# Optimization experiments

Measured on AMD Instinct MI355X. Metric: run time of the kernel, lower is better.

The kernel has to match this reference:

```python
import jax, jax.numpy as jnp
import numpy as np

B, S, C = 16, 512, 512
T = 4096  # mel_max_len


def setup_inputs() -> dict:
    key = jax.random.key(0)
    k1, k2 = jax.random.split(key)
    durations = jax.random.randint(k1, (B, S), 0, 16, dtype=jnp.int32)
    enc_out = jax.random.normal(k2, (B, S, C), dtype=jnp.float32)
    return {"durations": durations, "enc_out": enc_out, "mel_max_len": T}


def reference(durations, enc_out, mel_max_len):
    # regulate_len with pace=1.0 and fixed mel_max_len (jit-static output length)
    pace = 1.0
    dtype = enc_out.dtype
    reps = (durations.astype(jnp.float32) / pace + 0.5).astype(jnp.int32)  # [B,S]
    dec_lens = reps.sum(axis=1)  # [B]
    # padded cumulative sums: [B, S+1]
    reps_cumsum = jnp.concatenate(
        [jnp.zeros((reps.shape[0], 1), reps.dtype), jnp.cumsum(reps, axis=1)], axis=1
    ).astype(dtype)[:, None, :]  # [B,1,S+1]
    range_ = jnp.arange(mel_max_len, dtype=dtype)[None, :, None]  # [1,T,1]
    mult = ((reps_cumsum[:, :, :-1] <= range_) & (reps_cumsum[:, :, 1:] > range_)).astype(dtype)  # [B,T,S]
    enc_rep = jnp.einsum('bts,bsc->btc', mult, enc_out)  # [B,T,C]
    dec_lens = jnp.minimum(dec_lens, mel_max_len)
    return enc_rep, dec_lens, reps.astype(jnp.float32)
```

## Files before the change

### kernel.cpp

```cpp
#include <hip/hip_runtime.h>

#define B_ 16
#define S_ 512
#define C_ 512
#define T_ 4096

typedef float f32x4 __attribute__((ext_vector_type(4)));

__global__ void __launch_bounds__(S_) regulate_scan_map_kernel(
    const int* __restrict__ dur,
    int* __restrict__ map,
    float* __restrict__ dec_out,
    float* __restrict__ reps_out)
{
    const int b    = blockIdx.x;
    const int s    = threadIdx.x;
    const int lane = s & 63;
    const int wid  = s >> 6;

    __shared__ int wsum[8];

    const int rep = dur[b * S_ + s];
    reps_out[b * S_ + s] = (float)rep;

    int x = rep;
    #pragma unroll
    for (int off = 1; off < 64; off <<= 1) {
        int y = __shfl_up(x, off, 64);
        if (lane >= off) x += y;
    }
    if (lane == 63) wsum[wid] = x;
    __syncthreads();

    int prefix = 0, total = 0;
    #pragma unroll
    for (int w = 0; w < 8; ++w) {
        int v = wsum[w];
        if (w < wid) prefix += v;
        total += v;
    }

    const int incl = prefix + x;
    const int excl = incl - rep;

    int start = excl < T_ ? excl : T_;
    int end   = incl < T_ ? incl : T_;
    int* __restrict__ m = map + (size_t)b * T_;
    for (int t = start; t < end; ++t) m[t] = s;

    const int tot_c = total < T_ ? total : T_;
    for (int t = tot_c + s; t < T_; t += S_) m[t] = -1;

    if (s == 0) dec_out[b] = (float)tot_c;
}

__global__ void __launch_bounds__(256) regulate_gather_kernel(
    const float* __restrict__ enc,
    const int* __restrict__ map,
    float* __restrict__ out)
{
    const int lin     = blockIdx.x;
    const int per     = gridDim.x >> 3;
    const int logical = (lin & 7) * per + (lin >> 3);

    const int b      = logical >> 10;
    const int tchunk = logical & 1023;
    const int row    = threadIdx.x >> 6;
    const int lane   = threadIdx.x & 63;
    const int t      = (tchunk << 2) + row;

    const int s = map[(size_t)b * T_ + t];

    f32x4 v0 = (f32x4)(0.f), v1 = (f32x4)(0.f);
    if (s >= 0) {
        const f32x4* __restrict__ rp =
            (const f32x4*)(enc + ((size_t)b * S_ + (size_t)s) * C_);
        v0 = rp[lane];
        v1 = rp[lane + 64];
    }
    f32x4* __restrict__ orow =
        (f32x4*)(out + ((size_t)b * T_ + (size_t)t) * C_);
    __builtin_nontemporal_store(v0, orow + lane);
    __builtin_nontemporal_store(v1, orow + lane + 64);
}

extern "C" void kernel_launch(void* const* d_in, const int* in_sizes, int n_in,
                              void* d_out, int out_size, void* d_ws, size_t ws_size,
                              hipStream_t stream)
{
    const int*   dur = (const int*)d_in[0];
    const float* enc = (const float*)d_in[1];

    float* out      = (float*)d_out;
    float* enc_rep  = out;
    float* dec_out  = out + (size_t)B_ * T_ * C_;
    float* reps_out = dec_out + B_;

    int* map = (int*)d_ws;

    regulate_scan_map_kernel<<<B_, S_, 0, stream>>>(dur, map, dec_out, reps_out);
    regulate_gather_kernel<<<(B_ * T_) / 4, 256, 0, stream>>>(enc, map, enc_rep);
}
```

Baseline: 32.49 us.

## Fuse duration scan into gather kernel, recomputing prefix sums per block

Removes the separate scan/map kernel and the workspace map by having every gather block redo the 512-entry prefix scan over its batch's durations (two per thread) and build a 4-entry row-to-source map in LDS. This drops one kernel launch and the serialized scan-then-gather dependency, including the map write and read through global memory. In exchange each of the 16K blocks does redundant scan work and a block-wide barrier before issuing its loads. The durations are small and likely cache-resident.

```diff
diff --git a/kernel.cpp b/kernel.cpp
--- a/kernel.cpp
+++ b/kernel.cpp
@@ -7,23 +7,33 @@
 
 typedef float f32x4 __attribute__((ext_vector_type(4)));
 
-__global__ void __launch_bounds__(S_) regulate_scan_map_kernel(
+__global__ void __launch_bounds__(256) regulate_fused_kernel(
     const int* __restrict__ dur,
-    int* __restrict__ map,
+    const float* __restrict__ enc,
+    float* __restrict__ out,
     float* __restrict__ dec_out,
     float* __restrict__ reps_out)
 {
-    const int b    = blockIdx.x;
-    const int s    = threadIdx.x;
-    const int lane = s & 63;
-    const int wid  = s >> 6;
+    const int lin     = blockIdx.x;
+    const int logical = (lin & 7) * (gridDim.x >> 3) + (lin >> 3);
 
-    __shared__ int wsum[8];
+    const int b      = logical >> 10;
+    const int tchunk = logical & 1023;
+    const int t0     = tchunk << 2;
 
-    const int rep = dur[b * S_ + s];
-    reps_out[b * S_ + s] = (float)rep;
+    const int tid  = threadIdx.x;
+    const int lane = tid & 63;
+    const int wid  = tid >> 6;
 
-    int x = rep;
+    __shared__ int wsum[4];
+    __shared__ int lds_map[4];
+
+    if (tid < 4) lds_map[tid] = -1;
+
+    const int2 d  = *(const int2*)(dur + b * S_ + (tid << 1));
+    const int pair = d.x + d.y;
+
+    int x = pair;
     #pragma unroll
     for (int off = 1; off < 64; off <<= 1) {
         int y = __shfl_up(x, off, 64);
@@ -34,42 +44,32 @@
 
     int prefix = 0, total = 0;
     #pragma unroll
-    for (int w = 0; w < 8; ++w) {
+    for (int w = 0; w < 4; ++w) {
         int v = wsum[w];
         if (w < wid) prefix += v;
         total += v;
     }
 
-    const int incl = prefix + x;
-    const int excl = incl - rep;
+    const int incl_pair = prefix + x;
+    const int excl0 = incl_pair - pair;
+    const int incl0 = excl0 + d.x;
+    const int incl1 = incl_pair;
 
-    int start = excl < T_ ? excl : T_;
-    int end   = incl < T_ ? incl : T_;
-    int* __restrict__ m = map + (size_t)b * T_;
-    for (int t = start; t < end; ++t) m[t] = s;
+    #pragma unroll
+    for (int j = 0; j < 4; ++j) {
+        const int t = t0 + j;
+        if (t >= excl0 && t < incl0) lds_map[j] = (tid << 1);
+        if (t >= incl0 && t < incl1) lds_map[j] = (tid << 1) | 1;
+    }
 
-    const int tot_c = total < T_ ? total : T_;
-    for (int t = tot_c + s; t < T_; t += S_) m[t] = -1;
+    if (tchunk == 0) {
+        *(float2*)(reps_out + b * S_ + (tid << 1)) =
+            make_float2((float)d.x, (float)d.y);
+        if (tid == 0) dec_out[b] = (float)(total < T_ ? total : T_);
+    }
+    __syncthreads();
 
-    if (s == 0) dec_out[b] = (float)tot_c;
-}
-
-__global__ void __launch_bounds__(256) regulate_gather_kernel(
-    const float* __restrict__ enc,
-    const int* __restrict__ map,
-    float* __restrict__ out)
-{
-    const int lin     = blockIdx.x;
-    const int per     = gridDim.x >> 3;
-    const int logical = (lin & 7) * per + (lin >> 3);
-
-    const int b      = logical >> 10;
-    const int tchunk = logical & 1023;
-    const int row    = threadIdx.x >> 6;
-    const int lane   = threadIdx.x & 63;
-    const int t      = (tchunk << 2) + row;
-
-    const int s = map[(size_t)b * T_ + t];
+    const int s = lds_map[wid];
 
     f32x4 v0 = (f32x4)(0.f), v1 = (f32x4)(0.f);
     if (s >= 0) {
@@ -78,10 +78,10 @@
         v0 = rp[lane];
         v1 = rp[lane + 64];
     }
-    f32x4* __restrict__ orow =
-        (f32x4*)(out + ((size_t)b * T_ + (size_t)t) * C_);
-    __builtin_nontemporal_store(v0, orow + lane);
-    __builtin_nontemporal_store(v1, orow + lane + 64);
+    f32x4* __restrict__ op =
+        (f32x4*)(out + ((size_t)b * T_ + (size_t)(t0 + wid)) * C_);
+    __builtin_nontemporal_store(v0, op + lane);
+    __builtin_nontemporal_store(v1, op + lane + 64);
 }
 
 extern "C" void kernel_launch(void* const* d_in, const int* in_sizes, int n_in,
@@ -96,8 +96,6 @@
     float* dec_out  = out + (size_t)B_ * T_ * C_;
     float* reps_out = dec_out + B_;
 
-    int* map = (int*)d_ws;
-
-    regulate_scan_map_kernel<<<B_, S_, 0, stream>>>(dur, map, dec_out, reps_out);
-    regulate_gather_kernel<<<(B_ * T_) / 4, 256, 0, stream>>>(enc, map, enc_rep);
+    regulate_fused_kernel<<<(B_ * T_) / 4, 256, 0, stream>>>(
+        dur, enc, enc_rep, dec_out, reps_out);
 }
```

After: 27.70 us, median of 2. 1.17x faster.
